# Kernel optimization log

Measured on AMD Instinct MI355X. Metric: run time of the kernel, lower is better.

## Reference

```python
import jax, jax.numpy as jnp
import numpy as np

N = 100000       # nodes
E = 3200000      # edges
F_IN = 128       # num_node_features
DIM = 32         # hidden dim (fixed in Net1)
L = 3            # num_layers
C = 10           # num_classes


def setup_inputs() -> dict:
    key = jax.random.key(0)
    ks = jax.random.split(key, 16)
    x = jax.random.normal(ks[0], (N, F_IN), dtype=jnp.float32)
    src = jax.random.randint(ks[1], (E,), 0, N, dtype=jnp.int32)
    dst = jax.random.randint(ks[2], (E,), 0, N, dtype=jnp.int32)
    def glorot(k, shape):
        lim = np.sqrt(6.0 / (shape[0] + shape[1])).astype(np.float32)
        return jax.random.uniform(k, shape, jnp.float32, -lim, lim)
    dims = [F_IN, DIM, DIM]
    inp = {"x": x, "src": src, "dst": dst}
    for i in range(L):
        din = dims[i]
        inp[f"Wn{i}"] = glorot(ks[3 + 3 * i], (din, DIM))      # neighbor weight
        inp[f"bn{i}"] = jnp.zeros((DIM,), jnp.float32)          # neighbor bias
        inp[f"Ws{i}"] = glorot(ks[4 + 3 * i], (din, DIM))      # self weight (no bias)
    inp["fc_w"] = glorot(ks[13], (DIM * L + F_IN, C))
    inp["fc_b"] = jnp.zeros((C,), jnp.float32)
    return inp


def _graph_conv_wl(x, src, dst, Wn, bn, Ws):
    # GraphConv(norm='none'): transform then aggregate (sum over in-neighbors)
    h = x @ Wn                                   # [N, DIM]
    msg = h[src]                                 # [E, DIM] gather
    agg = jax.ops.segment_sum(msg, dst, num_segments=N)  # [N, DIM] scatter-add
    return agg + bn + x @ Ws


def reference(x, src, dst, Wn0, bn0, Ws0, Wn1, bn1, Ws1, Wn2, bn2, Ws2, fc_w, fc_b):
    params = [(Wn0, bn0, Ws0), (Wn1, bn1, Ws1), (Wn2, bn2, Ws2)]
    xs = [x]
    h = x
    for Wn, bn, Ws in params:
        h = jax.nn.relu(_graph_conv_wl(h, src, dst, Wn, bn, Ws))
        xs.append(h)
    h = jnp.concatenate(xs, axis=1)              # [N, 128 + 3*32]
    logits = h @ fc_w + fc_b                     # [N, C]
    return jax.nn.log_softmax(logits, axis=1)
```

## Files before the change

kernel.cpp:

```cpp
#include <hip/hip_runtime.h>
#include <cstdint>

#define NN 100000
#define EE 3200000
#define SB_BITS 8
#define SB_NODES (1 << SB_BITS)
#define NSB ((NN + SB_NODES - 1) / SB_NODES)
#define CAP 9216
#define CH 4096
#define EPT (CH / 256)
#define TRH ((NN + 63) / 64)

__device__ inline float4 add4(float4 a, float4 b) {
    return make_float4(a.x + b.x, a.y + b.y, a.z + b.z, a.w + b.w);
}

__device__ inline unsigned pk_bf2(float lo, float hi) {
    unsigned a = __float_as_uint(lo);
    unsigned b = __float_as_uint(hi);
    a = (a + 0x7FFFu + ((a >> 16) & 1u)) >> 16;
    b = (b + 0x7FFFu + ((b >> 16) & 1u)) & 0xFFFF0000u;
    return a | b;
}


__global__ void k_hist_sb(const int* __restrict__ dst, int* __restrict__ scnt) {
    __shared__ int h[NSB];
    for (int i = threadIdx.x; i < NSB; i += 256) h[i] = 0;
    __syncthreads();
    for (int e = blockIdx.x * 256 + threadIdx.x; e < EE; e += gridDim.x * 256)
        atomicAdd(&h[dst[e] >> SB_BITS], 1);
    __syncthreads();
    for (int i = threadIdx.x; i < NSB; i += 256) {
        int v = h[i];
        if (v) atomicAdd(&scnt[i], v);
    }
}

__global__ void k_scan_sb(const int* __restrict__ scnt,
                          int* __restrict__ sbptr, int* __restrict__ cursor) {
    __shared__ int sm[512];
    int i = threadIdx.x;
    int v0 = (i < NSB) ? scnt[i] : 0;
    int v1 = (i + 256 < NSB) ? scnt[i + 256] : 0;
    sm[i] = v0;
    sm[i + 256] = v1;
    __syncthreads();
    for (int o = 1; o < 512; o <<= 1) {
        int a0 = (i >= o) ? sm[i - o] : 0;
        int a1 = (i + 256 >= o) ? sm[i + 256 - o] : 0;
        __syncthreads();
        sm[i] += a0;
        sm[i + 256] += a1;
        __syncthreads();
    }
    if (i < NSB)       { sbptr[i]       = sm[i] - v0;       cursor[i]       = sm[i] - v0; }
    if (i + 256 < NSB) { sbptr[i + 256] = sm[i + 256] - v1; cursor[i + 256] = sm[i + 256] - v1; }
    if (i == 0) sbptr[NSB] = sm[511];
}

__global__ void k_split(const int* __restrict__ src, const int* __restrict__ dst,
                        int* __restrict__ cursor, int* __restrict__ out) {
    __shared__ int hist[512];
    __shared__ int lbase[NSB];
    __shared__ int gbase[NSB];
    __shared__ int buf[CH];
    __shared__ unsigned short keyb[CH];
    const int nchunks = (EE + CH - 1) / CH;
    for (int c = blockIdx.x; c < nchunks; c += gridDim.x) {
        int base = c * CH;
        int cnt = min(CH, EE - base);
        hist[threadIdx.x] = 0;
        hist[threadIdx.x + 256] = 0;
        __syncthreads();
        int words[EPT], ranks[EPT], keys[EPT];
        #pragma unroll
        for (int k = 0; k < EPT; ++k) {
            int idx = threadIdx.x + k * 256;
            if (idx < cnt) {
                int d = dst[base + idx];
                int s = src[base + idx];
                int key = d >> SB_BITS;
                words[k] = s | ((d & (SB_NODES - 1)) << 17);
                keys[k] = key;
                ranks[k] = atomicAdd(&hist[key], 1);
            } else keys[k] = -1;
        }
        __syncthreads();
        int i = threadIdx.x;
        int v0 = hist[i], v1 = hist[i + 256];
        for (int o = 1; o < 512; o <<= 1) {
            int a0 = (i >= o) ? hist[i - o] : 0;
            int a1 = (i + 256 >= o) ? hist[i + 256 - o] : 0;
            __syncthreads();
            hist[i] += a0;
            hist[i + 256] += a1;
            __syncthreads();
        }
        if (i < NSB) {
            lbase[i] = hist[i] - v0;
            gbase[i] = (v0 > 0) ? atomicAdd(&cursor[i], v0) : 0;
        }
        if (i + 256 < NSB) {
            lbase[i + 256] = hist[i + 256] - v1;
            gbase[i + 256] = (v1 > 0) ? atomicAdd(&cursor[i + 256], v1) : 0;
        }
        __syncthreads();
        #pragma unroll
        for (int k = 0; k < EPT; ++k) {
            if (keys[k] >= 0) {
                int p = lbase[keys[k]] + ranks[k];
                buf[p] = words[k];
                keyb[p] = (unsigned short)keys[k];
            }
        }
        __syncthreads();
        for (int j = threadIdx.x; j < cnt; j += 256) {
            int kk = keyb[j];
            out[gbase[kk] + (j - lbase[kk])] = buf[j];
        }
        __syncthreads();
    }
}

__global__ void k_sb_sort(const int* __restrict__ sbptr, const int* __restrict__ packed,
                          int* __restrict__ csr_src, int* __restrict__ rowptr) {
    __shared__ int hist[SB_NODES];
    __shared__ int lbuf[CAP];
    int b = blockIdx.x;
    int e0 = sbptr[b], e1 = sbptr[b + 1];
    int cnt = e1 - e0;
    hist[threadIdx.x] = 0;
    __syncthreads();
    for (int j = e0 + threadIdx.x; j < e1; j += 256)
        atomicAdd(&hist[(packed[j] >> 17) & (SB_NODES - 1)], 1);
    __syncthreads();
    int i = threadIdx.x;
    int v = hist[i];
    for (int o = 1; o < 256; o <<= 1) {
        int a = (i >= o) ? hist[i - o] : 0;
        __syncthreads();
        hist[i] += a;
        __syncthreads();
    }
    int excl = hist[i] - v;
    int node = (b << SB_BITS) + i;
    if (node < NN) rowptr[node] = e0 + excl;
    hist[i] = excl;
    if (b == 0 && i == 0) rowptr[NN] = EE;
    __syncthreads();
    if (cnt <= CAP) {
        for (int j = e0 + threadIdx.x; j < e1; j += 256) {
            int w = packed[j];
            int n = (w >> 17) & (SB_NODES - 1);
            int pos = atomicAdd(&hist[n], 1);
            lbuf[pos] = w & 0x1FFFF;
        }
        __syncthreads();
        for (int j = threadIdx.x; j < cnt; j += 256)
            csr_src[e0 + j] = lbuf[j];
    } else {
        for (int j = e0 + threadIdx.x; j < e1; j += 256) {
            int w = packed[j];
            int n = (w >> 17) & (SB_NODES - 1);
            int pos = atomicAdd(&hist[n], 1);
            csr_src[e0 + pos] = w & 0x1FFFF;
        }
    }
}


template <int DIN>
__global__ __launch_bounds__(64, 2) void k_transform(
        const float* __restrict__ h,
        const float* __restrict__ Wn,
        const float* __restrict__ Ws,
        const float* __restrict__ bn,
        unsigned* __restrict__ t_bf,
        float* __restrict__ hout) {
    const int half = (blockIdx.x >= TRH) ? 1 : 0;
    const int d0 = half * 16;
    const int node = (blockIdx.x - half * TRH) * 64 + threadIdx.x;
    if (node >= NN) return;
    const float* __restrict__ hr = h + (size_t)node * DIN;
    float accn[16], accs[16];
    #pragma unroll
    for (int d = 0; d < 16; ++d) { accn[d] = 0.f; accs[d] = 0.f; }
    constexpr int NK4 = DIN / 4;
    float4 f0 = *(const float4*)(hr);
    float4 f1 = *(const float4*)(hr + 4);
    float4 f2 = *(const float4*)(hr + 8);
    #pragma unroll 2
    for (int k4 = 0; k4 < NK4; ++k4) {
        float4 cur = f0;
        f0 = f1;
        f1 = f2;
        if (k4 + 3 < NK4) f2 = *(const float4*)(hr + (k4 + 3) * 4);
        float fj[4] = {cur.x, cur.y, cur.z, cur.w};
        #pragma unroll
        for (int j = 0; j < 4; ++j) {
            float fv = fj[j];
            const float* __restrict__ wn = Wn + (k4 * 4 + j) * 32 + d0;
            const float* __restrict__ ws = Ws + (k4 * 4 + j) * 32 + d0;
            #pragma unroll
            for (int d = 0; d < 16; ++d) {
                accn[d] = fmaf(fv, wn[d], accn[d]);
                accs[d] = fmaf(fv, ws[d], accs[d]);
            }
        }
    }
    unsigned tb[8];
    #pragma unroll
    for (int d = 0; d < 8; ++d) tb[d] = pk_bf2(accn[2 * d], accn[2 * d + 1]);
    unsigned* tp = t_bf + (size_t)node * 16 + half * 8;
    *(uint4*)(tp + 0) = make_uint4(tb[0], tb[1], tb[2], tb[3]);
    *(uint4*)(tp + 4) = make_uint4(tb[4], tb[5], tb[6], tb[7]);
    float* __restrict__ hp = hout + (size_t)node * 32 + d0;
    #pragma unroll
    for (int d = 0; d < 16; d += 4)
        *(float4*)(hp + d) = make_float4(accs[d] + bn[d0 + d], accs[d + 1] + bn[d0 + d + 1],
                                         accs[d + 2] + bn[d0 + d + 2], accs[d + 3] + bn[d0 + d + 3]);
}

__global__ void k_aggregate(const int* __restrict__ rowptr,
                            const int* __restrict__ csr_src,
                            const uint2* __restrict__ t2,
                            float4* __restrict__ hout4) {
    int node = blockIdx.x * 32 + (threadIdx.x >> 3);
    int q = threadIdx.x & 7;
    if (node >= NN) return;
    int j = rowptr[node];
    int end = rowptr[node + 1];
    float4 a0 = make_float4(0.f, 0.f, 0.f, 0.f);
    float4 a1 = a0, a2 = a0, a3 = a0;
    for (; j + 4 <= end; j += 4) {
        int s0 = csr_src[j];
        int s1 = csr_src[j + 1];
        int s2 = csr_src[j + 2];
        int s3 = csr_src[j + 3];
        uint2 u0 = t2[s0 * 8 + q];
        uint2 u1 = t2[s1 * 8 + q];
        uint2 u2 = t2[s2 * 8 + q];
        uint2 u3 = t2[s3 * 8 + q];
        a0.x += __uint_as_float(u0.x << 16); a0.y += __uint_as_float(u0.x & 0xFFFF0000u);
        a0.z += __uint_as_float(u0.y << 16); a0.w += __uint_as_float(u0.y & 0xFFFF0000u);
        a1.x += __uint_as_float(u1.x << 16); a1.y += __uint_as_float(u1.x & 0xFFFF0000u);
        a1.z += __uint_as_float(u1.y << 16); a1.w += __uint_as_float(u1.y & 0xFFFF0000u);
        a2.x += __uint_as_float(u2.x << 16); a2.y += __uint_as_float(u2.x & 0xFFFF0000u);
        a2.z += __uint_as_float(u2.y << 16); a2.w += __uint_as_float(u2.y & 0xFFFF0000u);
        a3.x += __uint_as_float(u3.x << 16); a3.y += __uint_as_float(u3.x & 0xFFFF0000u);
        a3.z += __uint_as_float(u3.y << 16); a3.w += __uint_as_float(u3.y & 0xFFFF0000u);
    }
    for (; j < end; ++j) {
        uint2 u = t2[csr_src[j] * 8 + q];
        a0.x += __uint_as_float(u.x << 16); a0.y += __uint_as_float(u.x & 0xFFFF0000u);
        a0.z += __uint_as_float(u.y << 16); a0.w += __uint_as_float(u.y & 0xFFFF0000u);
    }
    float4 s = add4(add4(a0, a1), add4(a2, a3));
    int idx = node * 8 + q;
    float4 h = hout4[idx];
    h.x = fmaxf(h.x + s.x, 0.f);
    h.y = fmaxf(h.y + s.y, 0.f);
    h.z = fmaxf(h.z + s.z, 0.f);
    h.w = fmaxf(h.w + s.w, 0.f);
    hout4[idx] = h;
}

__global__ void k_final(const float* __restrict__ x,
                        const float* __restrict__ h1,
                        const float* __restrict__ h2,
                        const float* __restrict__ h3,
                        const float* __restrict__ fc_w,
                        const float* __restrict__ fc_b,
                        float* __restrict__ out) {
    __shared__ float Wl[224 * 10];
    __shared__ float bl[10];
    for (int i = threadIdx.x; i < 224 * 10; i += blockDim.x) Wl[i] = fc_w[i];
    if (threadIdx.x < 10) bl[threadIdx.x] = fc_b[threadIdx.x];
    __syncthreads();
    int n = blockIdx.x * blockDim.x + threadIdx.x;
    if (n >= NN) return;
    float acc[10];
    #pragma unroll
    for (int c = 0; c < 10; ++c) acc[c] = bl[c];
    const float4* xr4 = (const float4*)(x + (size_t)n * 128);
    for (int j4 = 0; j4 < 32; ++j4) {
        float4 f = xr4[j4];
        #pragma unroll
        for (int c = 0; c < 10; ++c) acc[c] += f.x * Wl[(j4 * 4 + 0) * 10 + c];
        #pragma unroll
        for (int c = 0; c < 10; ++c) acc[c] += f.y * Wl[(j4 * 4 + 1) * 10 + c];
        #pragma unroll
        for (int c = 0; c < 10; ++c) acc[c] += f.z * Wl[(j4 * 4 + 2) * 10 + c];
        #pragma unroll
        for (int c = 0; c < 10; ++c) acc[c] += f.w * Wl[(j4 * 4 + 3) * 10 + c];
    }
    const float* hs[3] = {h1, h2, h3};
    for (int l = 0; l < 3; ++l) {
        const float4* hr4 = (const float4*)(hs[l] + (size_t)n * 32);
        const int base = 128 + l * 32;
        for (int j4 = 0; j4 < 8; ++j4) {
            float4 f = hr4[j4];
            #pragma unroll
            for (int c = 0; c < 10; ++c) acc[c] += f.x * Wl[(base + j4 * 4 + 0) * 10 + c];
            #pragma unroll
            for (int c = 0; c < 10; ++c) acc[c] += f.y * Wl[(base + j4 * 4 + 1) * 10 + c];
            #pragma unroll
            for (int c = 0; c < 10; ++c) acc[c] += f.z * Wl[(base + j4 * 4 + 2) * 10 + c];
            #pragma unroll
            for (int c = 0; c < 10; ++c) acc[c] += f.w * Wl[(base + j4 * 4 + 3) * 10 + c];
        }
    }
    float m = acc[0];
    #pragma unroll
    for (int c = 1; c < 10; ++c) m = fmaxf(m, acc[c]);
    float s = 0.f;
    #pragma unroll
    for (int c = 0; c < 10; ++c) s += __expf(acc[c] - m);
    float ls = __logf(s);
    #pragma unroll
    for (int c = 0; c < 10; ++c) out[n * 10 + c] = acc[c] - m - ls;
}

extern "C" void kernel_launch(void* const* d_in, const int* in_sizes, int n_in,
                              void* d_out, int out_size, void* d_ws, size_t ws_size,
                              hipStream_t stream) {
    const float* x   = (const float*)d_in[0];
    const int*   src = (const int*)d_in[1];
    const int*   dst = (const int*)d_in[2];
    const float* Wn[3] = {(const float*)d_in[3], (const float*)d_in[6], (const float*)d_in[9]};
    const float* bn[3] = {(const float*)d_in[4], (const float*)d_in[7], (const float*)d_in[10]};
    const float* Ws[3] = {(const float*)d_in[5], (const float*)d_in[8], (const float*)d_in[11]};
    const float* fc_w = (const float*)d_in[12];
    const float* fc_b = (const float*)d_in[13];
    float* out = (float*)d_out;

    char* w = (char*)d_ws;
    const size_t NF = (size_t)NN * 32;
    unsigned* t_bf = (unsigned*)w;              w += (size_t)NN * 16 * 4;
    float* h1  = (float*)w;                     w += NF * 4;
    float* h2  = (float*)w;                     w += NF * 4;
    float* h3  = (float*)w;                     w += NF * 4;
    int* csr_src = (int*)w;                     w += (size_t)EE * 4;
    int* scnt   = (int*)w;                      w += (size_t)NSB * 4;
    int* sbptr  = (int*)w;                      w += (size_t)(NSB + 1) * 4;
    int* cursor = (int*)w;                      w += (size_t)NSB * 4;
    int* rowptr = (int*)w;                      w += (size_t)(NN + 1) * 4;
    int* packed = (int*)h3;

    hipMemsetAsync(scnt, 0, (size_t)NSB * 4, stream);
    k_hist_sb<<<512, 256, 0, stream>>>(dst, scnt);
    k_scan_sb<<<1, 256, 0, stream>>>(scnt, sbptr, cursor);
    k_split<<<512, 256, 0, stream>>>(src, dst, cursor, packed);
    k_sb_sort<<<NSB, 256, 0, stream>>>(sbptr, packed, csr_src, rowptr);

    const int tr_blocks = 2 * TRH;
    const int ag_blocks = (NN + 31) / 32;
    k_transform<128><<<tr_blocks, 64, 0, stream>>>(x, Wn[0], Ws[0], bn[0], t_bf, h1);
    k_aggregate<<<ag_blocks, 256, 0, stream>>>(rowptr, csr_src, (const uint2*)t_bf, (float4*)h1);
    k_transform<32><<<tr_blocks, 64, 0, stream>>>(h1, Wn[1], Ws[1], bn[1], t_bf, h2);
    k_aggregate<<<ag_blocks, 256, 0, stream>>>(rowptr, csr_src, (const uint2*)t_bf, (float4*)h2);
    k_transform<32><<<tr_blocks, 64, 0, stream>>>(h2, Wn[2], Ws[2], bn[2], t_bf, h3);
    k_aggregate<<<ag_blocks, 256, 0, stream>>>(rowptr, csr_src, (const uint2*)t_bf, (float4*)h3);
    k_final<<<(NN + 255) / 256, 256, 0, stream>>>(x, h1, h2, h3, fc_w, fc_b, out);
}
```

Measured before the change: 432.9 us.

## Split transform K-dimension across four waves with shared-memory reduction

The node transform kernel now launches 256-thread blocks where each of four waves handles a quarter of the input features for the same 64 nodes. Partial sums from waves 1-3 are written to shared memory and reduced by wave 0, which then writes the bf16 neighbor transform and self term. Block halves are interleaved instead of split across the grid. This adds parallelism and latency hiding to the transform, at the cost of shared memory, a barrier, and idle waves during the epilogue.

```diff
diff --git a/kernel.cpp b/kernel.cpp
--- a/kernel.cpp
+++ b/kernel.cpp
@@ -171,37 +171,41 @@
 
 
 template <int DIN>
-__global__ __launch_bounds__(64, 2) void k_transform(
+__global__ __launch_bounds__(256, 4) void k_transform(
         const float* __restrict__ h,
         const float* __restrict__ Wn,
         const float* __restrict__ Ws,
         const float* __restrict__ bn,
         unsigned* __restrict__ t_bf,
         float* __restrict__ hout) {
-    const int half = (blockIdx.x >= TRH) ? 1 : 0;
+    __shared__ __align__(16) float part[3][32][64];
+    const int half = blockIdx.x & 1;
     const int d0 = half * 16;
-    const int node = (blockIdx.x - half * TRH) * 64 + threadIdx.x;
-    if (node >= NN) return;
-    const float* __restrict__ hr = h + (size_t)node * DIN;
+    const int tid = threadIdx.x & 63;
+    const int wv = __builtin_amdgcn_readfirstlane(threadIdx.x >> 6);
+    const int node = (blockIdx.x >> 1) * 64 + tid;
+    const bool valid = node < NN;
+    const float* __restrict__ hr = h + (size_t)(valid ? node : NN - 1) * DIN;
+    constexpr int NK4W = DIN / 16;
+    const int kb = wv * NK4W;
     float accn[16], accs[16];
     #pragma unroll
     for (int d = 0; d < 16; ++d) { accn[d] = 0.f; accs[d] = 0.f; }
-    constexpr int NK4 = DIN / 4;
-    float4 f0 = *(const float4*)(hr);
-    float4 f1 = *(const float4*)(hr + 4);
-    float4 f2 = *(const float4*)(hr + 8);
+    float4 f0 = *(const float4*)(hr + (kb + 0) * 4);
+    float4 f1 = *(const float4*)(hr + (kb + 1) * 4);
+    float4 f2 = (NK4W > 2) ? *(const float4*)(hr + (kb + 2) * 4) : f1;
     #pragma unroll 2
-    for (int k4 = 0; k4 < NK4; ++k4) {
+    for (int k4 = 0; k4 < NK4W; ++k4) {
         float4 cur = f0;
         f0 = f1;
         f1 = f2;
-        if (k4 + 3 < NK4) f2 = *(const float4*)(hr + (k4 + 3) * 4);
+        if (k4 + 3 < NK4W) f2 = *(const float4*)(hr + (kb + k4 + 3) * 4);
         float fj[4] = {cur.x, cur.y, cur.z, cur.w};
         #pragma unroll
         for (int j = 0; j < 4; ++j) {
             float fv = fj[j];
-            const float* __restrict__ wn = Wn + (k4 * 4 + j) * 32 + d0;
-            const float* __restrict__ ws = Ws + (k4 * 4 + j) * 32 + d0;
+            const float* __restrict__ wn = Wn + ((kb + k4) * 4 + j) * 32 + d0;
+            const float* __restrict__ ws = Ws + ((kb + k4) * 4 + j) * 32 + d0;
             #pragma unroll
             for (int d = 0; d < 16; ++d) {
                 accn[d] = fmaf(fv, wn[d], accn[d]);
@@ -209,17 +213,39 @@
             }
         }
     }
-    unsigned tb[8];
-    #pragma unroll
-    for (int d = 0; d < 8; ++d) tb[d] = pk_bf2(accn[2 * d], accn[2 * d + 1]);
-    unsigned* tp = t_bf + (size_t)node * 16 + half * 8;
-    *(uint4*)(tp + 0) = make_uint4(tb[0], tb[1], tb[2], tb[3]);
-    *(uint4*)(tp + 4) = make_uint4(tb[4], tb[5], tb[6], tb[7]);
-    float* __restrict__ hp = hout + (size_t)node * 32 + d0;
-    #pragma unroll
-    for (int d = 0; d < 16; d += 4)
-        *(float4*)(hp + d) = make_float4(accs[d] + bn[d0 + d], accs[d + 1] + bn[d0 + d + 1],
-                                         accs[d + 2] + bn[d0 + d + 2], accs[d + 3] + bn[d0 + d + 3]);
+    if (wv != 0) {
+        float* p = &part[wv - 1][0][0];
+        #pragma unroll
+        for (int d = 0; d < 16; ++d) {
+            p[d * 64 + tid]        = accn[d];
+            p[(16 + d) * 64 + tid] = accs[d];
+        }
+    }
+    __syncthreads();
+    if (wv == 0) {
+        #pragma unroll
+        for (int w = 0; w < 3; ++w) {
+            const float* p = &part[w][0][0];
+            #pragma unroll
+            for (int d = 0; d < 16; ++d) {
+                accn[d] += p[d * 64 + tid];
+                accs[d] += p[(16 + d) * 64 + tid];
+            }
+        }
+        if (valid) {
+            unsigned tb[8];
+            #pragma unroll
+            for (int d = 0; d < 8; ++d) tb[d] = pk_bf2(accn[2 * d], accn[2 * d + 1]);
+            unsigned* tp = t_bf + (size_t)node * 16 + half * 8;
+            *(uint4*)(tp + 0) = make_uint4(tb[0], tb[1], tb[2], tb[3]);
+            *(uint4*)(tp + 4) = make_uint4(tb[4], tb[5], tb[6], tb[7]);
+            float* __restrict__ hp = hout + (size_t)node * 32 + d0;
+            #pragma unroll
+            for (int d = 0; d < 16; d += 4)
+                *(float4*)(hp + d) = make_float4(accs[d] + bn[d0 + d], accs[d + 1] + bn[d0 + d + 1],
+                                                 accs[d + 2] + bn[d0 + d + 2], accs[d + 3] + bn[d0 + d + 3]);
+        }
+    }
 }
 
 __global__ void k_aggregate(const int* __restrict__ rowptr,
@@ -356,11 +382,11 @@
 
     const int tr_blocks = 2 * TRH;
     const int ag_blocks = (NN + 31) / 32;
-    k_transform<128><<<tr_blocks, 64, 0, stream>>>(x, Wn[0], Ws[0], bn[0], t_bf, h1);
+    k_transform<128><<<tr_blocks, 256, 0, stream>>>(x, Wn[0], Ws[0], bn[0], t_bf, h1);
     k_aggregate<<<ag_blocks, 256, 0, stream>>>(rowptr, csr_src, (const uint2*)t_bf, (float4*)h1);
-    k_transform<32><<<tr_blocks, 64, 0, stream>>>(h1, Wn[1], Ws[1], bn[1], t_bf, h2);
+    k_transform<32><<<tr_blocks, 256, 0, stream>>>(h1, Wn[1], Ws[1], bn[1], t_bf, h2);
     k_aggregate<<<ag_blocks, 256, 0, stream>>>(rowptr, csr_src, (const uint2*)t_bf, (float4*)h2);
-    k_transform<32><<<tr_blocks, 64, 0, stream>>>(h2, Wn[2], Ws[2], bn[2], t_bf, h3);
+    k_transform<32><<<tr_blocks, 256, 0, stream>>>(h2, Wn[2], Ws[2], bn[2], t_bf, h3);
     k_aggregate<<<ag_blocks, 256, 0, stream>>>(rowptr, csr_src, (const uint2*)t_bf, (float4*)h3);
     k_final<<<(NN + 255) / 256, 256, 0, stream>>>(x, h1, h2, h3, fc_w, fc_b, out);
 }
```

New measurement: 424.9 us. About the same (-1.8%).
